# Performance work log

Hardware: AMD Instinct MI355X
Metric: run time of the kernel (lower is better)

The kernel has to match this reference:

```python
import jax, jax.numpy as jnp
import numpy as np

# irreps = 128x0e + 64x1e + 32x2e  (dim = 128 + 64*3 + 32*5 = 480)
# hidden = 512x0e + 256x1e + 128x2e ; gate scalars = (256+128) x0e
N = 65536
M0, M1, M2 = 128, 64, 32          # input multiplicities per degree l=0,1,2
H0, H1, H2 = 512, 256, 128        # hidden multiplicities
G = H1 + H2                       # number of sigmoid gate scalars
EPS = 1e-8
S0 = float(np.sqrt(M0)); S1 = float(np.sqrt(M1)); S2 = float(np.sqrt(M2))
T0 = float(np.sqrt(H0)); T1 = float(np.sqrt(H1)); T2 = float(np.sqrt(H2))


def setup_inputs() -> dict:
    key = jax.random.key(0)
    ks = jax.random.split(key, 8)
    p = lambda k, shape: jax.random.normal(k, shape, dtype=jnp.float32)
    return dict(
        x=p(ks[0], (N, M0 + 3 * M1 + 5 * M2)),
        # SeperableLayerNorm affine params (weight per channel; bias only for scalars)
        nw0=jnp.ones((M0,), jnp.float32), nb0=jnp.zeros((M0,), jnp.float32),
        nw1=jnp.ones((M1,), jnp.float32), nw2=jnp.ones((M2,), jnp.float32),
        # lin1: irreps -> (hidden scalars + gates) 0e, hidden 1e, hidden 2e. e3nn fan-in norm.
        W0=p(ks[1], (M0, H0 + G)), b0=jnp.zeros((H0 + G,), jnp.float32),
        W1=p(ks[2], (M1, H1)), W2=p(ks[3], (M2, H2)),
        # lin2: gated hidden -> irreps
        V0=p(ks[4], (H0, M0)), c0=jnp.zeros((M0,), jnp.float32),
        V1=p(ks[5], (H1, M1)), V2=p(ks[6], (H2, M2)),
        alpha=jnp.float32(0.5),
    )


def _ffn(x, nw0, nb0, nw1, nw2, W0, b0, W1, W2, V0, c0, V1, V2, alpha):
    n = x.shape[0]
    x0 = x[:, :M0]                                   # [n, 128] scalars
    x1 = x[:, M0:M0 + 3 * M1].reshape(n, M1, 3)      # [n, 64, 3]
    x2 = x[:, M0 + 3 * M1:].reshape(n, M2, 5)        # [n, 32, 5]

    # --- SeperableLayerNorm (component norm, std_balance_degrees) ---
    # scalars: standard layer norm over scalar channels
    mu = jnp.mean(x0, axis=-1, keepdims=True)
    xc = x0 - mu
    y0 = xc * jax.lax.rsqrt(jnp.mean(xc * xc, axis=-1, keepdims=True) + EPS) * nw0 + nb0
    # l>0: RMS norm, each degree contributes equally (balance over degrees)
    s1 = jnp.mean(x1 * x1, axis=(1, 2))
    s2 = jnp.mean(x2 * x2, axis=(1, 2))
    inv = jax.lax.rsqrt(0.5 * (s1 + s2) + EPS)[:, None, None]
    y1 = x1 * inv * nw1[:, None]
    y2 = x2 * inv * nw2[:, None]

    # --- lin1 (e3nn Linear: per-degree block matmul, 1/sqrt(fan_in), bias on 0e) ---
    h0 = y0 @ W0 / S0 + b0                            # [n, 896]
    h1 = jnp.einsum('num,uw->nwm', y1, W1) / S1       # [n, 256, 3]
    h2 = jnp.einsum('num,uw->nwm', y2, W2) / S2       # [n, 128, 5]

    # --- Gate: silu on hidden scalars, sigmoid gates broadcast onto l>0 ---
    s = jax.nn.silu(h0[:, :H0])
    g = jax.nn.sigmoid(h0[:, H0:])
    z1 = h1 * g[:, :H1, None]
    z2 = h2 * g[:, H1:, None]

    # --- lin2 ---
    o0 = s @ V0 / T0 + c0
    o1 = jnp.einsum('num,uw->nwm', z1, V1) / T1
    o2 = jnp.einsum('num,uw->nwm', z2, V2) / T2
    dx = jnp.concatenate([o0, o1.reshape(n, -1), o2.reshape(n, -1)], axis=-1)
    return x + jnp.tanh(alpha) * dx


def reference(x, nw0, nb0, nw1, nw2, W0, b0, W1, W2, V0, c0, V1, V2, alpha):
    return _ffn(x, nw0, nb0, nw1, nw2, W0, b0, W1, W2, V0, c0, V1, V2, alpha)
```

## Files before the change

kernel.cpp:

```cpp
#include <hip/hip_runtime.h>
#include <stdint.h>

#define NROWS 65536
#define DCOL  480
#define RT    16

#define INV_S0 0.08838834764831845f
#define INV_S1 0.125f
#define INV_S2 0.17677669529663687f
#define INV_T0 0.044194173824159216f
#define INV_T1 0.0625f
#define INV_T2 0.08838834764831845f

#define OFF_W0T 0
#define OFF_W1T 114688
#define OFF_W2T 131072
#define OFF_V0T 135168
#define OFF_V1T 200704
#define OFF_V2T 217088
#define TOT_W   221184

typedef __attribute__((ext_vector_type(8))) short  short8;
typedef __attribute__((ext_vector_type(4))) float  floatx4;

__device__ __forceinline__ uint16_t f2bf(float x){
  uint32_t u = __builtin_bit_cast(uint32_t, x);
  return (uint16_t)((u + 0x8000u) >> 16);
}
__device__ __forceinline__ float bf2f(uint16_t h){
  return __builtin_bit_cast(float, (uint32_t)h << 16);
}

#define MFMA16(a,b,c) __builtin_amdgcn_mfma_f32_16x16x32_bf16((a),(b),(c),0,0,0)

__global__ __launch_bounds__(256)
void convert_weights(const float* __restrict__ W0, const float* __restrict__ W1,
                     const float* __restrict__ W2, const float* __restrict__ V0,
                     const float* __restrict__ V1, const float* __restrict__ V2,
                     uint16_t* __restrict__ wt)
{
  const int tid = blockIdx.x*256 + threadIdx.x;
  if (tid >= TOT_W) return;
  if (tid < OFF_W1T){
    const int i = tid;            const int n = i>>7, k = i&127;
    wt[tid] = f2bf(W0[(size_t)k*896 + n] * INV_S0);
  } else if (tid < OFF_W2T){
    const int i = tid - OFF_W1T;  const int n = i>>6, k = i&63;
    wt[tid] = f2bf(W1[(size_t)k*256 + n] * INV_S1);
  } else if (tid < OFF_V0T){
    const int i = tid - OFF_W2T;  const int n = i>>5, k = i&31;
    wt[tid] = f2bf(W2[(size_t)k*128 + n] * INV_S2);
  } else if (tid < OFF_V1T){
    const int i = tid - OFF_V0T;  const int n = i>>9, k = i&511;
    wt[tid] = f2bf(V0[(size_t)k*128 + n] * INV_T0);
  } else if (tid < OFF_V2T){
    const int i = tid - OFF_V1T;  const int n = i>>8, k = i&255;
    wt[tid] = f2bf(V1[(size_t)k*64 + n] * INV_T1);
  } else {
    const int i = tid - OFF_V2T;  const int n = i>>7, k = i&127;
    wt[tid] = f2bf(V2[(size_t)k*32 + n] * INV_T2);
  }
}

__global__ __launch_bounds__(512, 4)
void ffn_mfma(const float* __restrict__ x,  const float* __restrict__ nw0,
              const float* __restrict__ nb0,const float* __restrict__ nw1,
              const float* __restrict__ nw2,const float* __restrict__ b0,
              const float* __restrict__ c0, const float* __restrict__ alpha,
              const uint16_t* __restrict__ wt, float* __restrict__ out)
{
  __shared__ __align__(16) uint16_t pool[34304];

  uint16_t (*gbf )[392]      = (uint16_t (*)[392])     (pool);
  uint16_t (*y1bf)[16][72]   = (uint16_t (*)[16][72])  (pool + 6272);
  uint16_t (*z2bf)[16][136]  = (uint16_t (*)[16][136]) (pool + 9728);
  uint16_t (*z1bf)[16][264]  = (uint16_t (*)[16][264]) (pool + 20608);
  uint16_t (*y2bf)[16][40]   = (uint16_t (*)[16][40])  (pool + 20608);
  uint16_t (*sbf )[520]      = (uint16_t (*)[520])     (pool + 23808);
  uint16_t (*y0bf)[136]      = (uint16_t (*)[136])     (pool + 32128);

  const int t      = threadIdx.x;
  const int wave   = t >> 6, lane = t & 63;
  const int lane16 = lane & 15, quad = lane >> 4;
  const int row0   = blockIdx.x * RT;
  const float ta   = tanhf(alpha[0]);
  const floatx4 fz = {0.f,0.f,0.f,0.f};

  {
    float xv[2][8];
    const int rbase = wave*2;
    #pragma unroll
    for (int rr=0; rr<2; ++rr){
      const float* xr = x + (size_t)(row0 + rbase + rr)*DCOL;
      #pragma unroll
      for (int i=0;i<8;++i){ const int e = lane + i*64; xv[rr][i] = (e < DCOL) ? xr[e] : 0.f; }
    }
    float wA[8], wB[8]; int uu[8], mmv[8];
    #pragma unroll
    for (int i=0;i<8;++i){
      const int e = lane + i*64;
      if (e < 128){ uu[i]=e; mmv[i]=0; wA[i]=nw0[e]; wB[i]=nb0[e]; }
      else if (e < 320){ const int d=e-128; const int u=d/3; uu[i]=u; mmv[i]=d-3*u; wA[i]=nw1[u]; wB[i]=0.f; }
      else if (e < DCOL){ const int d=e-320; const int u=d/5; uu[i]=u; mmv[i]=d-5*u; wA[i]=nw2[u]; wB[i]=0.f; }
      else { uu[i]=0; mmv[i]=0; wA[i]=0.f; wB[i]=0.f; }
    }
    #pragma unroll
    for (int rr=0; rr<2; ++rr){
      const int r = rbase + rr;
      float s0  = xv[rr][0] + xv[rr][1];
      float s0q = xv[rr][0]*xv[rr][0] + xv[rr][1]*xv[rr][1];
      float q1  = xv[rr][2]*xv[rr][2] + xv[rr][3]*xv[rr][3] + xv[rr][4]*xv[rr][4];
      float q2  = xv[rr][5]*xv[rr][5] + xv[rr][6]*xv[rr][6] + xv[rr][7]*xv[rr][7];
      #pragma unroll
      for (int off=32; off>0; off>>=1){
        s0  += __shfl_xor(s0,  off);
        s0q += __shfl_xor(s0q, off);
        q1  += __shfl_xor(q1,  off);
        q2  += __shfl_xor(q2,  off);
      }
      const float mu   = s0 * (1.f/128.f);
      const float var  = s0q * (1.f/128.f) - mu*mu;
      const float rstd = rsqrtf(var + 1e-8f);
      const float inv  = rsqrtf(0.5f*(q1*(1.f/192.f) + q2*(1.f/160.f)) + 1e-8f);
      #pragma unroll
      for (int i=0;i<8;++i){
        const int e = lane + i*64;
        if (e < 128)       y0bf[r][e] = f2bf((xv[rr][i]-mu)*rstd*wA[i] + wB[i]);
        else if (e < 320)  y1bf[mmv[i]][r][uu[i]] = f2bf(xv[rr][i]*inv*wA[i]);
        else if (e < DCOL) y2bf[mmv[i]][r][uu[i]] = f2bf(xv[rr][i]*inv*wA[i]);
      }
    }
  }
  __syncthreads();

  {
    short8 a0[4];
    #pragma unroll
    for (int kk=0; kk<4; ++kk)
      a0[kk] = *(const short8*)&y0bf[lane16][kk*32 + quad*8];
    const uint16_t* W0t = wt + OFF_W0T;

    auto ldW0 = [&](int tile, short8* dst){
      #pragma unroll
      for (int kk=0;kk<4;++kk)
        dst[kk] = *(const short8*)(W0t + (size_t)(tile*16+lane16)*128 + kk*32 + quad*8);
    };
    auto h0_tile = [&](int tile, const short8* bfr){
      floatx4 acc = fz;
      #pragma unroll
      for (int kk=0;kk<4;++kk) acc = MFMA16(a0[kk], bfr[kk], acc);
      const int col  = tile*16 + lane16;
      const float bias = b0[col];
      #pragma unroll
      for (int r2=0; r2<4; ++r2){
        const int row = quad*4 + r2;
        const float h  = acc[r2] + bias;
        const float sg = 1.f/(1.f + __expf(-h));
        if (col < 512) sbf[row][col]       = f2bf(h*sg);
        else           gbf[row][col - 512] = f2bf(sg);
      }
    };

    short8 buf[2][4];
    ldW0(wave, buf[0]);
    #pragma unroll
    for (int it=0; it<7; ++it){
      const int cur = it & 1;
      if (it < 6) ldW0(wave + (it+1)*8, buf[cur^1]);
      h0_tile(wave + it*8, buf[cur]);
    }
  }
  __syncthreads();

  {
    const uint16_t* W2t = wt + OFF_W2T;
    const uint16_t* V0t = wt + OFF_V0T;
    const int col = wave*16 + lane16;
    const short8 b2 = *(const short8*)(W2t + (size_t)col*32 + quad*8);
    short8 a2[5];
    #pragma unroll
    for (int m=0;m<5;++m) a2[m] = *(const short8*)&y2bf[m][lane16][quad*8];
    float g2v[4], xra[4];
    #pragma unroll
    for (int r2=0;r2<4;++r2){
      g2v[r2] = bf2f(gbf[quad*4+r2][256+col]);
      xra[r2] = x[(size_t)(row0+quad*4+r2)*DCOL + col];
    }
    const float cc = c0[col];
    floatx4 acc = fz;
    #pragma unroll 4
    for (int kk=0; kk<16; ++kk){
      const short8 a = *(const short8*)&sbf[lane16][kk*32 + quad*8];
      const short8 b = *(const short8*)(V0t + (size_t)col*512 + kk*32 + quad*8);
      acc = MFMA16(a, b, acc);
    }
    #pragma unroll
    for (int m=0;m<5;++m){
      floatx4 h = MFMA16(a2[m], b2, fz);
      #pragma unroll
      for (int r2=0;r2<4;++r2)
        z2bf[m][quad*4+r2][col] = f2bf(h[r2]*g2v[r2]);
    }
    #pragma unroll
    for (int r2=0;r2<4;++r2)
      out[(size_t)(row0+quad*4+r2)*DCOL + col] = xra[r2] + ta*(acc[r2]+cc);
  }
  __syncthreads();

  {
    if (wave < 6){
      const uint16_t* W1t = wt + OFF_W1T;
      short8 a1[3][2];
      #pragma unroll
      for (int m=0;m<3;++m){
        a1[m][0] = *(const short8*)&y1bf[m][lane16][quad*8];
        a1[m][1] = *(const short8*)&y1bf[m][lane16][32 + quad*8];
      }
      const int nt    = (wave < 4) ? 3 : 2;
      const int tbase = (wave < 4) ? wave*3 : 12 + (wave-4)*2;
      #pragma unroll 1
      for (int tt=0; tt<nt; ++tt){
        const int col = (tbase+tt)*16 + lane16;
        const short8 b0f = *(const short8*)(W1t + (size_t)col*64 + quad*8);
        const short8 b1f = *(const short8*)(W1t + (size_t)col*64 + 32 + quad*8);
        float gv[4];
        #pragma unroll
        for (int r2=0;r2<4;++r2) gv[r2] = bf2f(gbf[quad*4+r2][col]);
        #pragma unroll
        for (int m=0;m<3;++m){
          floatx4 am = MFMA16(a1[m][0], b0f, fz);
          am = MFMA16(a1[m][1], b1f, am);
          #pragma unroll
          for (int r2=0;r2<4;++r2)
            z1bf[m][quad*4+r2][col] = f2bf(am[r2]*gv[r2]);
        }
      }
    } else {
      const uint16_t* V2t = wt + OFF_V2T;
      const int col = (wave-6)*16 + lane16;
      short8 ob[4];
      #pragma unroll
      for (int kk=0;kk<4;++kk)
        ob[kk] = *(const short8*)(V2t + (size_t)col*128 + kk*32 + quad*8);
      float xo[5][4];
      #pragma unroll
      for (int m=0;m<5;++m)
        #pragma unroll
        for (int r2=0;r2<4;++r2)
          xo[m][r2] = x[(size_t)(row0+quad*4+r2)*DCOL + 320 + col*5 + m];
      floatx4 am[5];
      #pragma unroll
      for (int m=0;m<5;++m){
        am[m] = fz;
        #pragma unroll
        for (int kk=0;kk<4;++kk){
          const short8 a = *(const short8*)&z2bf[m][lane16][kk*32 + quad*8];
          am[m] = MFMA16(a, ob[kk], am[m]);
        }
      }
      #pragma unroll
      for (int m=0;m<5;++m)
        #pragma unroll
        for (int r2=0;r2<4;++r2){
          const size_t idx = (size_t)(row0+quad*4+r2)*DCOL + 320 + col*5 + m;
          out[idx] = xo[m][r2] + ta*am[m][r2];
        }
    }
  }
  __syncthreads();

  {
    const uint16_t* V1t = wt + OFF_V1T;
    const int col = (wave & 3)*16 + lane16;
    short8 vb[8];
    #pragma unroll
    for (int kk=0;kk<8;++kk)
      vb[kk] = *(const short8*)(V1t + (size_t)col*256 + kk*32 + quad*8);
    if (wave < 4){
      float xr0[4], xr2[4];
      #pragma unroll
      for (int r2=0;r2<4;++r2){
        const size_t base = (size_t)(row0+quad*4+r2)*DCOL + 128 + col*3;
        xr0[r2] = x[base + 0];
        xr2[r2] = x[base + 2];
      }
      floatx4 am0 = fz, am2 = fz;
      #pragma unroll
      for (int kk=0;kk<8;++kk){
        const short8 f0 = *(const short8*)&z1bf[0][lane16][kk*32 + quad*8];
        const short8 f2 = *(const short8*)&z1bf[2][lane16][kk*32 + quad*8];
        am0 = MFMA16(f0, vb[kk], am0);
        am2 = MFMA16(f2, vb[kk], am2);
      }
      #pragma unroll
      for (int r2=0;r2<4;++r2){
        const size_t base = (size_t)(row0+quad*4+r2)*DCOL + 128 + col*3;
        out[base + 0] = xr0[r2] + ta*am0[r2];
        out[base + 2] = xr2[r2] + ta*am2[r2];
      }
    } else {
      float xr1[4];
      #pragma unroll
      for (int r2=0;r2<4;++r2)
        xr1[r2] = x[(size_t)(row0+quad*4+r2)*DCOL + 128 + col*3 + 1];
      floatx4 am1 = fz;
      #pragma unroll
      for (int kk=0;kk<8;++kk){
        const short8 f1 = *(const short8*)&z1bf[1][lane16][kk*32 + quad*8];
        am1 = MFMA16(f1, vb[kk], am1);
      }
      #pragma unroll
      for (int r2=0;r2<4;++r2)
        out[(size_t)(row0+quad*4+r2)*DCOL + 128 + col*3 + 1] = xr1[r2] + ta*am1[r2];
    }
  }
}

extern "C" void kernel_launch(void* const* d_in, const int* in_sizes, int n_in,
                              void* d_out, int out_size, void* d_ws, size_t ws_size,
                              hipStream_t stream) {
  const float* x   = (const float*)d_in[0];
  const float* nw0 = (const float*)d_in[1];
  const float* nb0 = (const float*)d_in[2];
  const float* nw1 = (const float*)d_in[3];
  const float* nw2 = (const float*)d_in[4];
  const float* W0  = (const float*)d_in[5];
  const float* b0  = (const float*)d_in[6];
  const float* W1  = (const float*)d_in[7];
  const float* W2  = (const float*)d_in[8];
  const float* V0  = (const float*)d_in[9];
  const float* c0  = (const float*)d_in[10];
  const float* V1  = (const float*)d_in[11];
  const float* V2  = (const float*)d_in[12];
  const float* al  = (const float*)d_in[13];
  uint16_t* wt = (uint16_t*)d_ws;

  convert_weights<<<dim3((TOT_W + 255)/256), dim3(256), 0, stream>>>(
      W0, W1, W2, V0, V1, V2, wt);
  ffn_mfma<<<dim3(NROWS/RT), dim3(512), 0, stream>>>(
      x, nw0, nb0, nw1, nw2, b0, c0, al, wt, (float*)d_out);
}
```

Baseline: 429.9 us.

## Widen block to 12 waves and rebalance per-stage work across waves

Raises the block from 8 to 12 waves (768 threads) and redistributes every stage: the layernorm row split, the h0 tile assignment (5 or 4 tiles per wave), separate waves for the V0 and W2 stages, and one degree component per wave in the final V1 stage. It also removes the software double-buffered W0 loads in favour of a plain loop. The goal is more waves in flight per CU and better load balance between stages, at the cost of a tighter per-thread register budget under the new launch bounds and losing the explicit load prefetch.

```diff
diff --git a/kernel.cpp b/kernel.cpp
--- a/kernel.cpp
+++ b/kernel.cpp
@@ -62,7 +62,7 @@
   }
 }
 
-__global__ __launch_bounds__(512, 4)
+__global__ __launch_bounds__(768, 6)
 void ffn_mfma(const float* __restrict__ x,  const float* __restrict__ nw0,
               const float* __restrict__ nb0,const float* __restrict__ nw1,
               const float* __restrict__ nw2,const float* __restrict__ b0,
@@ -87,14 +87,7 @@
   const floatx4 fz = {0.f,0.f,0.f,0.f};
 
   {
-    float xv[2][8];
-    const int rbase = wave*2;
-    #pragma unroll
-    for (int rr=0; rr<2; ++rr){
-      const float* xr = x + (size_t)(row0 + rbase + rr)*DCOL;
-      #pragma unroll
-      for (int i=0;i<8;++i){ const int e = lane + i*64; xv[rr][i] = (e < DCOL) ? xr[e] : 0.f; }
-    }
+    const int nr = (wave < 4) ? 2 : 1;
     float wA[8], wB[8]; int uu[8], mmv[8];
     #pragma unroll
     for (int i=0;i<8;++i){
@@ -106,11 +99,16 @@
     }
     #pragma unroll
     for (int rr=0; rr<2; ++rr){
-      const int r = rbase + rr;
-      float s0  = xv[rr][0] + xv[rr][1];
-      float s0q = xv[rr][0]*xv[rr][0] + xv[rr][1]*xv[rr][1];
-      float q1  = xv[rr][2]*xv[rr][2] + xv[rr][3]*xv[rr][3] + xv[rr][4]*xv[rr][4];
-      float q2  = xv[rr][5]*xv[rr][5] + xv[rr][6]*xv[rr][6] + xv[rr][7]*xv[rr][7];
+      if (rr >= nr) break;
+      const int r = (rr == 0) ? wave : wave + 12;
+      const float* xr = x + (size_t)(row0 + r)*DCOL;
+      float xv[8];
+      #pragma unroll
+      for (int i=0;i<8;++i){ const int e = lane + i*64; xv[i] = (e < DCOL) ? xr[e] : 0.f; }
+      float s0  = xv[0] + xv[1];
+      float s0q = xv[0]*xv[0] + xv[1]*xv[1];
+      float q1  = xv[2]*xv[2] + xv[3]*xv[3] + xv[4]*xv[4];
+      float q2  = xv[5]*xv[5] + xv[6]*xv[6] + xv[7]*xv[7];
       #pragma unroll
       for (int off=32; off>0; off>>=1){
         s0  += __shfl_xor(s0,  off);
@@ -125,9 +123,9 @@
       #pragma unroll
       for (int i=0;i<8;++i){
         const int e = lane + i*64;
-        if (e < 128)       y0bf[r][e] = f2bf((xv[rr][i]-mu)*rstd*wA[i] + wB[i]);
-        else if (e < 320)  y1bf[mmv[i]][r][uu[i]] = f2bf(xv[rr][i]*inv*wA[i]);
-        else if (e < DCOL) y2bf[mmv[i]][r][uu[i]] = f2bf(xv[rr][i]*inv*wA[i]);
+        if (e < 128)       y0bf[r][e] = f2bf((xv[i]-mu)*rstd*wA[i] + wB[i]);
+        else if (e < 320)  y1bf[mmv[i]][r][uu[i]] = f2bf(xv[i]*inv*wA[i]);
+        else if (e < DCOL) y2bf[mmv[i]][r][uu[i]] = f2bf(xv[i]*inv*wA[i]);
       }
     }
   }
@@ -139,16 +137,17 @@
     for (int kk=0; kk<4; ++kk)
       a0[kk] = *(const short8*)&y0bf[lane16][kk*32 + quad*8];
     const uint16_t* W0t = wt + OFF_W0T;
-
-    auto ldW0 = [&](int tile, short8* dst){
-      #pragma unroll
-      for (int kk=0;kk<4;++kk)
-        dst[kk] = *(const short8*)(W0t + (size_t)(tile*16+lane16)*128 + kk*32 + quad*8);
-    };
-    auto h0_tile = [&](int tile, const short8* bfr){
+    const int base = (wave < 8) ? wave*5 : 40 + (wave-8)*4;
+    const int nt   = (wave < 8) ? 5 : 4;
+    #pragma unroll 1
+    for (int it=0; it<nt; ++it){
+      const int tile = base + it;
       floatx4 acc = fz;
       #pragma unroll
-      for (int kk=0;kk<4;++kk) acc = MFMA16(a0[kk], bfr[kk], acc);
+      for (int kk=0;kk<4;++kk){
+        const short8 b = *(const short8*)(W0t + (size_t)(tile*16+lane16)*128 + kk*32 + quad*8);
+        acc = MFMA16(a0[kk], b, acc);
+      }
       const int col  = tile*16 + lane16;
       const float bias = b0[col];
       #pragma unroll
@@ -159,56 +158,55 @@
         if (col < 512) sbf[row][col]       = f2bf(h*sg);
         else           gbf[row][col - 512] = f2bf(sg);
       }
-    };
-
-    short8 buf[2][4];
-    ldW0(wave, buf[0]);
-    #pragma unroll
-    for (int it=0; it<7; ++it){
-      const int cur = it & 1;
-      if (it < 6) ldW0(wave + (it+1)*8, buf[cur^1]);
-      h0_tile(wave + it*8, buf[cur]);
     }
   }
   __syncthreads();
 
   {
-    const uint16_t* W2t = wt + OFF_W2T;
-    const uint16_t* V0t = wt + OFF_V0T;
-    const int col = wave*16 + lane16;
-    const short8 b2 = *(const short8*)(W2t + (size_t)col*32 + quad*8);
-    short8 a2[5];
-    #pragma unroll
-    for (int m=0;m<5;++m) a2[m] = *(const short8*)&y2bf[m][lane16][quad*8];
-    float g2v[4], xra[4];
-    #pragma unroll
-    for (int r2=0;r2<4;++r2){
-      g2v[r2] = bf2f(gbf[quad*4+r2][256+col]);
-      xra[r2] = x[(size_t)(row0+quad*4+r2)*DCOL + col];
-    }
-    const float cc = c0[col];
-    floatx4 acc = fz;
-    #pragma unroll 4
-    for (int kk=0; kk<16; ++kk){
-      const short8 a = *(const short8*)&sbf[lane16][kk*32 + quad*8];
-      const short8 b = *(const short8*)(V0t + (size_t)col*512 + kk*32 + quad*8);
-      acc = MFMA16(a, b, acc);
-    }
-    #pragma unroll
-    for (int m=0;m<5;++m){
-      floatx4 h = MFMA16(a2[m], b2, fz);
+    if (wave < 8){
+      const uint16_t* V0t = wt + OFF_V0T;
+      const int col = wave*16 + lane16;
+      float xra[4];
       #pragma unroll
       for (int r2=0;r2<4;++r2)
-        z2bf[m][quad*4+r2][col] = f2bf(h[r2]*g2v[r2]);
-    }
-    #pragma unroll
-    for (int r2=0;r2<4;++r2)
-      out[(size_t)(row0+quad*4+r2)*DCOL + col] = xra[r2] + ta*(acc[r2]+cc);
+        xra[r2] = x[(size_t)(row0+quad*4+r2)*DCOL + col];
+      const float cc = c0[col];
+      floatx4 acc = fz;
+      #pragma unroll 4
+      for (int kk=0; kk<16; ++kk){
+        const short8 a = *(const short8*)&sbf[lane16][kk*32 + quad*8];
+        const short8 b = *(const short8*)(V0t + (size_t)col*512 + kk*32 + quad*8);
+        acc = MFMA16(a, b, acc);
+      }
+      #pragma unroll
+      for (int r2=0;r2<4;++r2)
+        out[(size_t)(row0+quad*4+r2)*DCOL + col] = xra[r2] + ta*(acc[r2]+cc);
+    } else {
+      const uint16_t* W2t = wt + OFF_W2T;
+      short8 a2[5];
+      #pragma unroll
+      for (int m=0;m<5;++m) a2[m] = *(const short8*)&y2bf[m][lane16][quad*8];
+      #pragma unroll
+      for (int tt=0; tt<2; ++tt){
+        const int col = (2*(wave-8)+tt)*16 + lane16;
+        const short8 b2 = *(const short8*)(W2t + (size_t)col*32 + quad*8);
+        float g2v[4];
+        #pragma unroll
+        for (int r2=0;r2<4;++r2) g2v[r2] = bf2f(gbf[quad*4+r2][256+col]);
+        #pragma unroll
+        for (int m=0;m<5;++m){
+          floatx4 h = MFMA16(a2[m], b2, fz);
+          #pragma unroll
+          for (int r2=0;r2<4;++r2)
+            z2bf[m][quad*4+r2][col] = f2bf(h[r2]*g2v[r2]);
+        }
+      }
+    }
   }
   __syncthreads();
 
   {
-    if (wave < 6){
+    if (wave < 10){
       const uint16_t* W1t = wt + OFF_W1T;
       short8 a1[3][2];
       #pragma unroll
@@ -216,10 +214,11 @@
         a1[m][0] = *(const short8*)&y1bf[m][lane16][quad*8];
         a1[m][1] = *(const short8*)&y1bf[m][lane16][32 + quad*8];
       }
-      const int nt    = (wave < 4) ? 3 : 2;
-      const int tbase = (wave < 4) ? wave*3 : 12 + (wave-4)*2;
-      #pragma unroll 1
-      for (int tt=0; tt<nt; ++tt){
+      const int nt    = (wave < 6) ? 2 : 1;
+      const int tbase = (wave < 6) ? 2*wave : 12 + (wave-6);
+      #pragma unroll
+      for (int tt=0; tt<2; ++tt){
+        if (tt >= nt) break;
         const int col = (tbase+tt)*16 + lane16;
         const short8 b0f = *(const short8*)(W1t + (size_t)col*64 + quad*8);
         const short8 b1f = *(const short8*)(W1t + (size_t)col*64 + 32 + quad*8);
@@ -237,7 +236,7 @@
       }
     } else {
       const uint16_t* V2t = wt + OFF_V2T;
-      const int col = (wave-6)*16 + lane16;
+      const int col = (wave-10)*16 + lane16;
       short8 ob[4];
       #pragma unroll
       for (int kk=0;kk<4;++kk)
@@ -271,48 +270,25 @@
 
   {
     const uint16_t* V1t = wt + OFF_V1T;
+    const int m   = wave >> 2;
     const int col = (wave & 3)*16 + lane16;
     short8 vb[8];
     #pragma unroll
     for (int kk=0;kk<8;++kk)
       vb[kk] = *(const short8*)(V1t + (size_t)col*256 + kk*32 + quad*8);
-    if (wave < 4){
-      float xr0[4], xr2[4];
-      #pragma unroll
-      for (int r2=0;r2<4;++r2){
-        const size_t base = (size_t)(row0+quad*4+r2)*DCOL + 128 + col*3;
-        xr0[r2] = x[base + 0];
-        xr2[r2] = x[base + 2];
-      }
-      floatx4 am0 = fz, am2 = fz;
-      #pragma unroll
-      for (int kk=0;kk<8;++kk){
-        const short8 f0 = *(const short8*)&z1bf[0][lane16][kk*32 + quad*8];
-        const short8 f2 = *(const short8*)&z1bf[2][lane16][kk*32 + quad*8];
-        am0 = MFMA16(f0, vb[kk], am0);
-        am2 = MFMA16(f2, vb[kk], am2);
-      }
-      #pragma unroll
-      for (int r2=0;r2<4;++r2){
-        const size_t base = (size_t)(row0+quad*4+r2)*DCOL + 128 + col*3;
-        out[base + 0] = xr0[r2] + ta*am0[r2];
-        out[base + 2] = xr2[r2] + ta*am2[r2];
-      }
-    } else {
-      float xr1[4];
-      #pragma unroll
-      for (int r2=0;r2<4;++r2)
-        xr1[r2] = x[(size_t)(row0+quad*4+r2)*DCOL + 128 + col*3 + 1];
-      floatx4 am1 = fz;
-      #pragma unroll
-      for (int kk=0;kk<8;++kk){
-        const short8 f1 = *(const short8*)&z1bf[1][lane16][kk*32 + quad*8];
-        am1 = MFMA16(f1, vb[kk], am1);
-      }
-      #pragma unroll
-      for (int r2=0;r2<4;++r2)
-        out[(size_t)(row0+quad*4+r2)*DCOL + 128 + col*3 + 1] = xr1[r2] + ta*am1[r2];
-    }
+    float xr[4];
+    #pragma unroll
+    for (int r2=0;r2<4;++r2)
+      xr[r2] = x[(size_t)(row0+quad*4+r2)*DCOL + 128 + col*3 + m];
+    floatx4 am = fz;
+    #pragma unroll
+    for (int kk=0;kk<8;++kk){
+      const short8 f = *(const short8*)&z1bf[m][lane16][kk*32 + quad*8];
+      am = MFMA16(f, vb[kk], am);
+    }
+    #pragma unroll
+    for (int r2=0;r2<4;++r2)
+      out[(size_t)(row0+quad*4+r2)*DCOL + 128 + col*3 + m] = xr[r2] + ta*am[r2];
   }
 }
 
@@ -337,6 +313,6 @@
 
   convert_weights<<<dim3((TOT_W + 255)/256), dim3(256), 0, stream>>>(
       W0, W1, W2, V0, V1, V2, wt);
-  ffn_mfma<<<dim3(NROWS/RT), dim3(512), 0, stream>>>(
+  ffn_mfma<<<dim3(NROWS/RT), dim3(768), 0, stream>>>(
       x, nw0, nb0, nw1, nw2, b0, c0, al, wt, (float*)d_out);
 }
```

New measurement: 445.7 us. 1.04x slower.
